# Kernel optimization log

Hardware: AMD Instinct MI355X
Metric: run time of the kernel (lower is better)

Reference implementation:

```python
import jax, jax.numpy as jnp
import numpy as np

B, L, KDIM, QDIM, ADIM, ODIM, H = 4, 1024, 1024, 1024, 1024, 1024, 16
DK = ADIM // H
SCALE = float(np.sqrt(DK))
NEG_INF = float(np.finfo(np.float32).min)


def setup_inputs() -> dict:
    key = jax.random.key(0)
    ks = jax.random.split(key, 12)
    s = 0.02
    return {
        "key": jax.random.normal(ks[0], (B, L, KDIM), jnp.float32),
        "value": jax.random.normal(ks[1], (B, L, KDIM), jnp.float32),
        "query": jax.random.normal(ks[2], (B, L, QDIM), jnp.float32),
        "mask": jax.random.randint(ks[3], (B, L, L), 0, 2, jnp.int32),
        "Wk": jax.random.normal(ks[4], (ADIM, KDIM), jnp.float32) * s,
        "bk": jnp.zeros((ADIM,), jnp.float32),
        "Wv": jax.random.normal(ks[5], (ADIM, KDIM), jnp.float32) * s,
        "bv": jnp.zeros((ADIM,), jnp.float32),
        "Wq": jax.random.normal(ks[6], (ADIM, QDIM), jnp.float32) * s,
        "bq": jnp.zeros((ADIM,), jnp.float32),
        "Wo": jax.random.normal(ks[7], (ODIM, ADIM), jnp.float32) * s,
        "bo": jnp.zeros((ODIM,), jnp.float32),
    }


def reference(key, value, query, mask, Wk, bk, Wv, bv, Wq, bq, Wo, bo):
    bs, klen = key.shape[0], key.shape[1]
    qlen = query.shape[1]
    # projections -> [B, len, H, d_k]
    k = (key @ Wk.T + bk).reshape(bs, klen, H, DK)
    v = (value @ Wv.T + bv).reshape(bs, klen, H, DK)
    q = (query @ Wq.T + bq).reshape(bs, qlen, H, DK)
    # attention energy [B, qlen, klen, H]
    e = jnp.einsum('bihd,bjhd->bijh', q, k) / SCALE
    m = mask[:, :, :, None]  # [B,q,k,1] broadcasts over heads
    e = jnp.where(m == 0, NEG_INF, e)
    aw = jax.nn.softmax(e, axis=2)  # softmax over klen
    cv = jnp.einsum('bijh,bjhd->bihd', aw, v).reshape(bs, qlen, ADIM)
    cv = cv @ Wo.T + bo
    return cv, jnp.transpose(aw, (0, 3, 1, 2))  # [B,H,q,k]
```

## Files before the change

kernel.cpp:

```cpp
#include <hip/hip_runtime.h>
#include <hip/hip_bf16.h>

typedef __attribute__((ext_vector_type(8))) __bf16 bf16x8;
typedef __attribute__((ext_vector_type(8))) short short8;
typedef __attribute__((ext_vector_type(4))) short s16x4;
typedef __attribute__((ext_vector_type(4))) float f32x4;

#define LN 1024
#define NH 16
#define DKH 64

__device__ __forceinline__ short f2bf(float f) {
    unsigned u = __builtin_bit_cast(unsigned, f);
    u = u + 0x7fffu + ((u >> 16) & 1u);
    return (short)(u >> 16);
}
__device__ __forceinline__ float bf2f(short s) {
    return __builtin_bit_cast(float, ((unsigned)(unsigned short)s) << 16);
}

__device__ __forceinline__ void gl_lds16(const short* g, short* l) {
    __builtin_amdgcn_global_load_lds(
        (const __attribute__((address_space(1))) void*)g,
        (__attribute__((address_space(3))) void*)l, 16, 0, 0);
}

__global__ __launch_bounds__(256) void cvt_all(
    const float* __restrict__ q, const float* __restrict__ k, const float* __restrict__ v,
    const float* __restrict__ wq, const float* __restrict__ wk,
    const float* __restrict__ wv, const float* __restrict__ wo,
    short* __restrict__ dq, short* __restrict__ dk, short* __restrict__ dv,
    short* __restrict__ dwq, short* __restrict__ dwk,
    short* __restrict__ dwv, short* __restrict__ dwo)
{
    int bid = blockIdx.x;
    const float* s; short* d; int base;
    if      (bid < 2048) { s = q;  d = dq;  base = bid; }
    else if (bid < 4096) { s = k;  d = dk;  base = bid - 2048; }
    else if (bid < 6144) { s = v;  d = dv;  base = bid - 4096; }
    else if (bid < 6656) { s = wq; d = dwq; base = bid - 6144; }
    else if (bid < 7168) { s = wk; d = dwk; base = bid - 6656; }
    else if (bid < 7680) { s = wv; d = dwv; base = bid - 7168; }
    else                 { s = wo; d = dwo; base = bid - 7680; }
    int i = base * 256 + threadIdx.x;
    f32x4 a = ((const f32x4*)s)[i * 2];
    f32x4 b = ((const f32x4*)s)[i * 2 + 1];
    short8 o;
    #pragma unroll
    for (int j = 0; j < 4; ++j) { o[j] = f2bf(a[j]); o[4 + j] = f2bf(b[j]); }
    ((short8*)d)[i] = o;
}

__global__ __launch_bounds__(256) void mask_bits_kernel(
    const int* __restrict__ mask, unsigned long long* __restrict__ bits)
{
    const int i = blockIdx.x;
    const int b = blockIdx.y;
    const int q = threadIdx.x >> 6;
    const int lane = threadIdx.x & 63;
    const int* mp = &mask[((size_t)b * LN + i) * LN + q * 256 + lane * 4];
    int4 mv = *(const int4*)mp;
    unsigned long long b0 = __ballot(mv.x != 0);
    unsigned long long b1 = __ballot(mv.y != 0);
    unsigned long long b2 = __ballot(mv.z != 0);
    unsigned long long b3 = __ballot(mv.w != 0);
    if (lane == 0) {
        unsigned long long* o = &bits[(((size_t)b * LN + i) * 4 + q) * 4];
        o[0] = b0; o[1] = b1; o[2] = b2; o[3] = b3;
    }
}

template<int MODE>
__device__ __forceinline__ void gemm_body(
    const short* __restrict__ A, const short* __restrict__ Bt,
    const float* __restrict__ bias, void* __restrict__ Cp,
    int m0, int n0, int N, int K, short* lA, short* lB)
{
    const int tid = threadIdx.x;
    const int lane = tid & 63;
    const int wid = tid >> 6;
    const int wr = wid >> 1, wc = wid & 1;
    const int lr = lane & 15, lg = lane >> 4;

    int srow[2], skc[2];
    #pragma unroll
    for (int p = 0; p < 2; ++p) {
        int ch = p * 256 + wid * 64 + lane;
        srow[p] = ch >> 3;
        skc[p] = (((ch & 7) ^ (srow[p] & 7))) * 8;
    }

    f32x4 acc[2][2] = {};

    for (int k0 = 0; k0 < K; k0 += 64) {
        #pragma unroll
        for (int p = 0; p < 2; ++p) {
            short* dstA = &lA[(p * 256 + wid * 64) * 8];
            short* dstB = &lB[(p * 256 + wid * 64) * 8];
            gl_lds16(A  + (size_t)(m0 + srow[p]) * K + k0 + skc[p], dstA);
            gl_lds16(Bt + (size_t)(n0 + srow[p]) * K + k0 + skc[p], dstB);
        }
        __syncthreads();
        bf16x8 af[2][2], bfr[2][2];
        #pragma unroll
        for (int kh = 0; kh < 2; ++kh) {
            #pragma unroll
            for (int m = 0; m < 2; ++m) {
                int arow = wr * 32 + m * 16 + lr;
                af[kh][m] = *(const bf16x8*)&lA[arow * 64 + (((kh * 4 + lg) ^ (arow & 7)) * 8)];
            }
            #pragma unroll
            for (int n = 0; n < 2; ++n) {
                int brow = wc * 32 + n * 16 + lr;
                bfr[kh][n] = *(const bf16x8*)&lB[brow * 64 + (((kh * 4 + lg) ^ (brow & 7)) * 8)];
            }
        }
        #pragma unroll
        for (int kh = 0; kh < 2; ++kh)
            #pragma unroll
            for (int m = 0; m < 2; ++m)
                #pragma unroll
                for (int n = 0; n < 2; ++n)
                    acc[m][n] = __builtin_amdgcn_mfma_f32_16x16x32_bf16(af[kh][m], bfr[kh][n], acc[m][n], 0, 0, 0);
        __syncthreads();
    }

    #pragma unroll
    for (int m = 0; m < 2; ++m)
        #pragma unroll
        for (int n = 0; n < 2; ++n) {
            int col = n0 + wc * 32 + n * 16 + lr;
            float bb = bias[col];
            if (MODE == 1) {
                int row = m0 + wr * 32 + m * 16 + lg * 4;
                int bb_i = row >> 10, tok = row & 1023;
                int hh = col >> 6, dd = col & 63;
                s16x4 o;
                #pragma unroll
                for (int r = 0; r < 4; ++r) o[r] = f2bf(acc[m][n][r] + bb);
                *(s16x4*)&((short*)Cp)[((size_t)((bb_i * NH + hh) * DKH) + dd) * LN + tok] = o;
            } else {
                #pragma unroll
                for (int r = 0; r < 4; ++r) {
                    int row = m0 + wr * 32 + m * 16 + lg * 4 + r;
                    float v = acc[m][n][r] + bb;
                    if (MODE == 2) ((float*)Cp)[(size_t)row * N + col] = v;
                    else           ((short*)Cp)[(size_t)row * N + col] = f2bf(v);
                }
            }
        }
}

__global__ __launch_bounds__(256) void gemm_vq(
    const short* __restrict__ vin, const short* __restrict__ qin,
    const short* __restrict__ wv, const short* __restrict__ wq,
    const float* __restrict__ bv, const float* __restrict__ bq,
    short* __restrict__ vT, short* __restrict__ q_bf)
{
    __shared__ short lA[64 * 64];
    __shared__ short lB[64 * 64];
    const int m0 = blockIdx.y * 64, n0 = blockIdx.x * 64;
    if (blockIdx.z == 0)
        gemm_body<1>(vin, wv, bv, vT, m0, n0, 1024, 1024, lA, lB);
    else
        gemm_body<0>(qin, wq, bq, q_bf, m0, n0, 1024, 1024, lA, lB);
}

__global__ __launch_bounds__(256) void gemm_bf(
    const short* __restrict__ A, const short* __restrict__ Bt,
    const float* __restrict__ bias, short* __restrict__ C)
{
    __shared__ short lA[64 * 64];
    __shared__ short lB[64 * 64];
    gemm_body<0>(A, Bt, bias, C, blockIdx.y * 64, blockIdx.x * 64, 1024, 1024, lA, lB);
}

__global__ __launch_bounds__(256) void gemm_out(
    const short* __restrict__ A, const short* __restrict__ Bt,
    const float* __restrict__ bias, float* __restrict__ C)
{
    __shared__ short lA[64 * 64];
    __shared__ short lB[64 * 64];
    gemm_body<2>(A, Bt, bias, C, blockIdx.y * 64, blockIdx.x * 64, 1024, 1024, lA, lB);
}

__global__ __launch_bounds__(256, 2) void attn_kernel(
    const short* __restrict__ qb, const short* __restrict__ kb,
    const short* __restrict__ vT, const unsigned long long* __restrict__ mb,
    float* __restrict__ aw, short* __restrict__ cv)
{
    __shared__ short p_lds[32 * 1024];
    __shared__ float redbuf[4][32];

    const int bid = blockIdx.x;
    const int swz = (bid & 7) * 256 + (bid >> 3);
    const int i0 = (swz & 31) * 32;
    const int h = (swz >> 5) & 15;
    const int b = swz >> 9;

    const int tid = threadIdx.x;
    const int lane = tid & 63;
    const int w = tid >> 6;
    const int lr = lane & 15, lg = lane >> 4;

    unsigned long long Bm[2][4];
    #pragma unroll
    for (int g = 0; g < 2; ++g)
        #pragma unroll
        for (int r = 0; r < 4; ++r)
            Bm[g][r] = mb[(((size_t)b * LN + i0 + g * 16 + lg * 4 + r) * 4 + w) * 4 + (lr & 3)] >> (lr >> 2);

    bf16x8 a0[2], a1[2];
    #pragma unroll
    for (int g = 0; g < 2; ++g) {
        const short* qp = &qb[((size_t)b * LN + i0 + g * 16 + lr) * 1024 + h * 64 + lg * 8];
        a0[g] = *(const bf16x8*)qp;
        a1[g] = *(const bf16x8*)(qp + 32);
    }

    f32x4 acc[2][16];
    #pragma unroll
    for (int g = 0; g < 2; ++g)
        #pragma unroll
        for (int jf = 0; jf < 16; ++jf) acc[g][jf] = f32x4{0.f, 0.f, 0.f, 0.f};

    const size_t krow_base = (size_t)b * LN;
    #pragma unroll
    for (int jf = 0; jf < 16; ++jf) {
        int j0f = w * 256 + jf * 16;
        const short* kp = &kb[(krow_base + j0f + lr) * 1024 + h * 64 + lg * 8];
        bf16x8 b0 = *(const bf16x8*)kp;
        bf16x8 b1 = *(const bf16x8*)(kp + 32);
        acc[0][jf] = __builtin_amdgcn_mfma_f32_16x16x32_bf16(a0[0], b0, acc[0][jf], 0, 0, 0);
        acc[0][jf] = __builtin_amdgcn_mfma_f32_16x16x32_bf16(a1[0], b1, acc[0][jf], 0, 0, 0);
        acc[1][jf] = __builtin_amdgcn_mfma_f32_16x16x32_bf16(a0[1], b0, acc[1][jf], 0, 0, 0);
        acc[1][jf] = __builtin_amdgcn_mfma_f32_16x16x32_bf16(a1[1], b1, acc[1][jf], 0, 0, 0);
    }

    float ps[2][4] = {};
    #pragma unroll
    for (int g = 0; g < 2; ++g)
        #pragma unroll
        for (int jf = 0; jf < 16; ++jf)
            #pragma unroll
            for (int r = 0; r < 4; ++r) {
                float p = ((Bm[g][r] >> (jf * 4)) & 1ULL) ? __expf(acc[g][jf][r] * 0.125f) : 0.0f;
                acc[g][jf][r] = p;
                ps[g][r] += p;
            }

    #pragma unroll
    for (int g = 0; g < 2; ++g)
        #pragma unroll
        for (int r = 0; r < 4; ++r) {
            for (int off = 1; off < 16; off <<= 1) ps[g][r] += __shfl_xor(ps[g][r], off, 64);
        }
    if (lr == 0) {
        #pragma unroll
        for (int g = 0; g < 2; ++g)
            #pragma unroll
            for (int r = 0; r < 4; ++r) redbuf[w][g * 16 + lg * 4 + r] = ps[g][r];
    }

    #pragma unroll
    for (int g = 0; g < 2; ++g)
        #pragma unroll
        for (int jf = 0; jf < 16; ++jf) {
            int j = w * 256 + jf * 16 + lr;
            #pragma unroll
            for (int r = 0; r < 4; ++r) {
                int row = g * 16 + lg * 4 + r;
                int byte = (row * 2048 + j * 2) ^ ((row & 7) << 4);
                *(short*)((char*)p_lds + byte) = f2bf(acc[g][jf][r]);
            }
        }
    __syncthreads();

    {
        const int arow = tid >> 3;
        const int ac0 = tid & 7;
        float s = redbuf[0][arow] + redbuf[1][arow] + redbuf[2][arow] + redbuf[3][arow];
        float ainv = 1.0f / s;
        float* awr = aw + ((size_t)(b * NH + h) * LN + i0 + arow) * LN;
        const int abase = arow * 2048;
        const int aswz = (arow & 7) << 4;
        #pragma unroll
        for (int it = 0; it < 16; ++it) {
            int k = ac0 + it * 8;
            int byte = (abase + k * 16) ^ aswz;
            short8 pv = *(const short8*)((char*)p_lds + byte);
            f32x4 o0, o1;
            #pragma unroll
            for (int j = 0; j < 4; ++j) {
                o0[j] = bf2f(pv[j]) * ainv;
                o1[j] = bf2f(pv[4 + j]) * ainv;
            }
            *(f32x4*)&awr[k * 8] = o0;
            *(f32x4*)&awr[k * 8 + 4] = o1;
        }
    }

    float inv[2][4];
    #pragma unroll
    for (int g = 0; g < 2; ++g)
        #pragma unroll
        for (int r = 0; r < 4; ++r) {
            float s = redbuf[0][g * 16 + lg * 4 + r];
            for (int ww = 1; ww < 4; ++ww) s += redbuf[ww][g * 16 + lg * 4 + r];
            inv[g][r] = 1.0f / s;
        }

    f32x4 accA[2] = {}, accB[2] = {};
    const int d0 = w * 16;
    const short* vrow = vT + ((size_t)((b * NH + h) * DKH) + d0 + lr) * LN;
    #pragma unroll
    for (int ks = 0; ks < 32; ks += 2) {
        bf16x8 vb0 = *(const bf16x8*)&vrow[ks * 32 + lg * 8];
        bf16x8 vb1 = *(const bf16x8*)&vrow[(ks + 1) * 32 + lg * 8];
        #pragma unroll
        for (int g = 0; g < 2; ++g) {
            int row = g * 16 + lr;
            int byte0 = (row * 2048 + (ks * 32 + lg * 8) * 2) ^ ((row & 7) << 4);
            int byte1 = (row * 2048 + ((ks + 1) * 32 + lg * 8) * 2) ^ ((row & 7) << 4);
            bf16x8 pa0 = *(const bf16x8*)((char*)p_lds + byte0);
            bf16x8 pa1 = *(const bf16x8*)((char*)p_lds + byte1);
            accA[g] = __builtin_amdgcn_mfma_f32_16x16x32_bf16(pa0, vb0, accA[g], 0, 0, 0);
            accB[g] = __builtin_amdgcn_mfma_f32_16x16x32_bf16(pa1, vb1, accB[g], 0, 0, 0);
        }
    }
    #pragma unroll
    for (int g = 0; g < 2; ++g)
        #pragma unroll
        for (int r = 0; r < 4; ++r) {
            int irow = i0 + g * 16 + lg * 4 + r;
            cv[((size_t)b * LN + irow) * 1024 + h * 64 + d0 + lr] = f2bf((accA[g][r] + accB[g][r]) * inv[g][r]);
        }
}

extern "C" void kernel_launch(void* const* d_in, const int* in_sizes, int n_in,
                              void* d_out, int out_size, void* d_ws, size_t ws_size,
                              hipStream_t stream) {
    (void)in_sizes; (void)n_in; (void)out_size; (void)ws_size;
    const float* key   = (const float*)d_in[0];
    const float* value = (const float*)d_in[1];
    const float* query = (const float*)d_in[2];
    const int*   mask  = (const int*)d_in[3];
    const float* Wk = (const float*)d_in[4];
    const float* bk = (const float*)d_in[5];
    const float* Wv = (const float*)d_in[6];
    const float* bv = (const float*)d_in[7];
    const float* Wq = (const float*)d_in[8];
    const float* bq = (const float*)d_in[9];
    const float* Wo = (const float*)d_in[10];
    const float* bo = (const float*)d_in[11];

    float* out_cv = (float*)d_out;
    float* out_aw = out_cv + (size_t)4096 * 1024;

    unsigned long long* mbits_g = (unsigned long long*)out_cv;
    short* q_bf = (short*)((char*)d_out + (size_t)(1u << 19));

    const size_t MB = 1u << 20;
    char* ws = (char*)d_ws;
    short* qin  = (short*)(ws + 0 * MB);   short* k_bf  = qin;
    short* kin  = (short*)(ws + 8 * MB);   short* cv_bf = kin;
    short* vin  = (short*)(ws + 16 * MB);
    short* wq   = (short*)(ws + 24 * MB);
    short* wk   = (short*)(ws + 26 * MB);
    short* wv   = (short*)(ws + 28 * MB);
    short* wo   = (short*)(ws + 30 * MB);
    short* vT   = (short*)(ws + 32 * MB);

    dim3 blk(256);
    cvt_all<<<dim3(8192), blk, 0, stream>>>(
        query, key, value, Wq, Wk, Wv, Wo,
        qin, kin, vin, wq, wk, wv, wo);
    mask_bits_kernel<<<dim3(1024, 4), blk, 0, stream>>>(mask, mbits_g);

    gemm_vq<<<dim3(16, 64, 2), blk, 0, stream>>>(vin, qin, wv, wq, bv, bq, vT, q_bf);
    gemm_bf<<<dim3(16, 64), blk, 0, stream>>>(kin, wk, bk, k_bf);
    attn_kernel<<<dim3(2048), blk, 0, stream>>>(q_bf, k_bf, vT, mbits_g, out_aw, cv_bf);
    gemm_out<<<dim3(16, 64), blk, 0, stream>>>(cv_bf, wo, bo, out_cv);
}
```

Baseline: 203.7 us.

## Double-buffer GEMM LDS tiles and merge conversion with mask-bit packing kernel

```diff
diff --git a/kernel.cpp b/kernel.cpp
--- a/kernel.cpp
+++ b/kernel.cpp
@@ -25,48 +25,48 @@
         (__attribute__((address_space(3))) void*)l, 16, 0, 0);
 }
 
-__global__ __launch_bounds__(256) void cvt_all(
+__global__ __launch_bounds__(256) void prep_all(
     const float* __restrict__ q, const float* __restrict__ k, const float* __restrict__ v,
     const float* __restrict__ wq, const float* __restrict__ wk,
     const float* __restrict__ wv, const float* __restrict__ wo,
     short* __restrict__ dq, short* __restrict__ dk, short* __restrict__ dv,
     short* __restrict__ dwq, short* __restrict__ dwk,
-    short* __restrict__ dwv, short* __restrict__ dwo)
+    short* __restrict__ dwv, short* __restrict__ dwo,
+    const int* __restrict__ mask, unsigned long long* __restrict__ bits)
 {
     int bid = blockIdx.x;
-    const float* s; short* d; int base;
-    if      (bid < 2048) { s = q;  d = dq;  base = bid; }
-    else if (bid < 4096) { s = k;  d = dk;  base = bid - 2048; }
-    else if (bid < 6144) { s = v;  d = dv;  base = bid - 4096; }
-    else if (bid < 6656) { s = wq; d = dwq; base = bid - 6144; }
-    else if (bid < 7168) { s = wk; d = dwk; base = bid - 6656; }
-    else if (bid < 7680) { s = wv; d = dwv; base = bid - 7168; }
-    else                 { s = wo; d = dwo; base = bid - 7680; }
-    int i = base * 256 + threadIdx.x;
-    f32x4 a = ((const f32x4*)s)[i * 2];
-    f32x4 b = ((const f32x4*)s)[i * 2 + 1];
-    short8 o;
-    #pragma unroll
-    for (int j = 0; j < 4; ++j) { o[j] = f2bf(a[j]); o[4 + j] = f2bf(b[j]); }
-    ((short8*)d)[i] = o;
-}
-
-__global__ __launch_bounds__(256) void mask_bits_kernel(
-    const int* __restrict__ mask, unsigned long long* __restrict__ bits)
-{
-    const int i = blockIdx.x;
-    const int b = blockIdx.y;
-    const int q = threadIdx.x >> 6;
-    const int lane = threadIdx.x & 63;
-    const int* mp = &mask[((size_t)b * LN + i) * LN + q * 256 + lane * 4];
-    int4 mv = *(const int4*)mp;
-    unsigned long long b0 = __ballot(mv.x != 0);
-    unsigned long long b1 = __ballot(mv.y != 0);
-    unsigned long long b2 = __ballot(mv.z != 0);
-    unsigned long long b3 = __ballot(mv.w != 0);
-    if (lane == 0) {
-        unsigned long long* o = &bits[(((size_t)b * LN + i) * 4 + q) * 4];
-        o[0] = b0; o[1] = b1; o[2] = b2; o[3] = b3;
+    if (bid < 8192) {
+        const float* s; short* d; int base;
+        if      (bid < 2048) { s = q;  d = dq;  base = bid; }
+        else if (bid < 4096) { s = k;  d = dk;  base = bid - 2048; }
+        else if (bid < 6144) { s = v;  d = dv;  base = bid - 4096; }
+        else if (bid < 6656) { s = wq; d = dwq; base = bid - 6144; }
+        else if (bid < 7168) { s = wk; d = dwk; base = bid - 6656; }
+        else if (bid < 7680) { s = wv; d = dwv; base = bid - 7168; }
+        else                 { s = wo; d = dwo; base = bid - 7680; }
+        int i = base * 256 + threadIdx.x;
+        f32x4 a = ((const f32x4*)s)[i * 2];
+        f32x4 b = ((const f32x4*)s)[i * 2 + 1];
+        short8 o;
+        #pragma unroll
+        for (int j = 0; j < 4; ++j) { o[j] = f2bf(a[j]); o[4 + j] = f2bf(b[j]); }
+        ((short8*)d)[i] = o;
+    } else {
+        int mid = bid - 8192;
+        const int i = mid & 1023;
+        const int b = mid >> 10;
+        const int qq = threadIdx.x >> 6;
+        const int lane = threadIdx.x & 63;
+        const int* mp = &mask[((size_t)b * LN + i) * LN + qq * 256 + lane * 4];
+        int4 mv = *(const int4*)mp;
+        unsigned long long b0 = __ballot(mv.x != 0);
+        unsigned long long b1 = __ballot(mv.y != 0);
+        unsigned long long b2 = __ballot(mv.z != 0);
+        unsigned long long b3 = __ballot(mv.w != 0);
+        if (lane == 0) {
+            unsigned long long* o = &bits[(((size_t)b * LN + i) * 4 + qq) * 4];
+            o[0] = b0; o[1] = b1; o[2] = b2; o[3] = b3;
+        }
     }
 }
 
@@ -91,28 +91,42 @@
     }
 
     f32x4 acc[2][2] = {};
-
-    for (int k0 = 0; k0 < K; k0 += 64) {
-        #pragma unroll
-        for (int p = 0; p < 2; ++p) {
-            short* dstA = &lA[(p * 256 + wid * 64) * 8];
-            short* dstB = &lB[(p * 256 + wid * 64) * 8];
-            gl_lds16(A  + (size_t)(m0 + srow[p]) * K + k0 + skc[p], dstA);
-            gl_lds16(Bt + (size_t)(n0 + srow[p]) * K + k0 + skc[p], dstB);
-        }
-        __syncthreads();
+    const int NT = K >> 6;
+
+    #pragma unroll
+    for (int p = 0; p < 2; ++p) {
+        gl_lds16(A  + (size_t)(m0 + srow[p]) * K + skc[p], &lA[(p * 256 + wid * 64) * 8]);
+        gl_lds16(Bt + (size_t)(n0 + srow[p]) * K + skc[p], &lB[(p * 256 + wid * 64) * 8]);
+    }
+    __syncthreads();
+
+    for (int t = 0; t < NT; ++t) {
+        const int cur = t & 1;
+        if (t + 1 < NT) {
+            const int nb = cur ^ 1;
+            const int k0 = (t + 1) << 6;
+            #pragma unroll
+            for (int p = 0; p < 2; ++p) {
+                gl_lds16(A  + (size_t)(m0 + srow[p]) * K + k0 + skc[p],
+                         &lA[nb * 4096 + (p * 256 + wid * 64) * 8]);
+                gl_lds16(Bt + (size_t)(n0 + srow[p]) * K + k0 + skc[p],
+                         &lB[nb * 4096 + (p * 256 + wid * 64) * 8]);
+            }
+        }
+        const short* cA = &lA[cur * 4096];
+        const short* cB = &lB[cur * 4096];
         bf16x8 af[2][2], bfr[2][2];
         #pragma unroll
         for (int kh = 0; kh < 2; ++kh) {
             #pragma unroll
             for (int m = 0; m < 2; ++m) {
                 int arow = wr * 32 + m * 16 + lr;
-                af[kh][m] = *(const bf16x8*)&lA[arow * 64 + (((kh * 4 + lg) ^ (arow & 7)) * 8)];
+                af[kh][m] = *(const bf16x8*)&cA[arow * 64 + (((kh * 4 + lg) ^ (arow & 7)) * 8)];
             }
             #pragma unroll
             for (int n = 0; n < 2; ++n) {
                 int brow = wc * 32 + n * 16 + lr;
-                bfr[kh][n] = *(const bf16x8*)&lB[brow * 64 + (((kh * 4 + lg) ^ (brow & 7)) * 8)];
+                bfr[kh][n] = *(const bf16x8*)&cB[brow * 64 + (((kh * 4 + lg) ^ (brow & 7)) * 8)];
             }
         }
         #pragma unroll
@@ -157,31 +171,31 @@
     const float* __restrict__ bv, const float* __restrict__ bq,
     short* __restrict__ vT, short* __restrict__ q_bf)
 {
-    __shared__ short lA[64 * 64];
-    __shared__ short lB[64 * 64];
+    __shared__ short lA[2][64 * 64];
+    __shared__ short lB[2][64 * 64];
     const int m0 = blockIdx.y * 64, n0 = blockIdx.x * 64;
     if (blockIdx.z == 0)
-        gemm_body<1>(vin, wv, bv, vT, m0, n0, 1024, 1024, lA, lB);
+        gemm_body<1>(vin, wv, bv, vT, m0, n0, 1024, 1024, &lA[0][0], &lB[0][0]);
     else
-        gemm_body<0>(qin, wq, bq, q_bf, m0, n0, 1024, 1024, lA, lB);
+        gemm_body<0>(qin, wq, bq, q_bf, m0, n0, 1024, 1024, &lA[0][0], &lB[0][0]);
 }
 
 __global__ __launch_bounds__(256) void gemm_bf(
     const short* __restrict__ A, const short* __restrict__ Bt,
     const float* __restrict__ bias, short* __restrict__ C)
 {
-    __shared__ short lA[64 * 64];
-    __shared__ short lB[64 * 64];
-    gemm_body<0>(A, Bt, bias, C, blockIdx.y * 64, blockIdx.x * 64, 1024, 1024, lA, lB);
+    __shared__ short lA[2][64 * 64];
+    __shared__ short lB[2][64 * 64];
+    gemm_body<0>(A, Bt, bias, C, blockIdx.y * 64, blockIdx.x * 64, 1024, 1024, &lA[0][0], &lB[0][0]);
 }
 
 __global__ __launch_bounds__(256) void gemm_out(
     const short* __restrict__ A, const short* __restrict__ Bt,
     const float* __restrict__ bias, float* __restrict__ C)
 {
-    __shared__ short lA[64 * 64];
-    __shared__ short lB[64 * 64];
-    gemm_body<2>(A, Bt, bias, C, blockIdx.y * 64, blockIdx.x * 64, 1024, 1024, lA, lB);
+    __shared__ short lA[2][64 * 64];
+    __shared__ short lB[2][64 * 64];
+    gemm_body<2>(A, Bt, bias, C, blockIdx.y * 64, blockIdx.x * 64, 1024, 1024, &lA[0][0], &lB[0][0]);
 }
 
 __global__ __launch_bounds__(256, 2) void attn_kernel(
@@ -372,10 +386,10 @@
     short* vT   = (short*)(ws + 32 * MB);
 
     dim3 blk(256);
-    cvt_all<<<dim3(8192), blk, 0, stream>>>(
+    prep_all<<<dim3(12288), blk, 0, stream>>>(
         query, key, value, Wq, Wk, Wv, Wo,
-        qin, kin, vin, wq, wk, wv, wo);
-    mask_bits_kernel<<<dim3(1024, 4), blk, 0, stream>>>(mask, mbits_g);
+        qin, kin, vin, wq, wk, wv, wo,
+        mask, mbits_g);
 
     gemm_vq<<<dim3(16, 64, 2), blk, 0, stream>>>(vin, qin, wv, wq, bv, bq, vT, q_bf);
     gemm_bf<<<dim3(16, 64), blk, 0, stream>>>(kin, wk, bk, k_bf);
```

Result: slower. 208.9 us (+2.6%).
